# Kernel tuning notes

Measured on AMD Instinct MI355X. Metric: run time of the kernel, lower is better.

The kernel has to match this reference:

```python
import jax, jax.numpy as jnp
import numpy as np

B, N, D = 16, 96, 128
NUM_TOKENS, NUM_CLASSES = 14, 10
NUM_ROUNDS = 5


def setup_inputs() -> dict:
    key = jax.random.key(0)
    ks = jax.random.split(key, 8)
    def lin(k, fan_in, shape):
        return (jax.random.normal(k, shape, jnp.float32) / np.sqrt(fan_in)).astype(jnp.float32)
    return {
        "tok": jax.random.randint(ks[0], (B, N), 0, NUM_TOKENS),
        "A": jax.random.uniform(ks[1], (B, N, N), jnp.float32),
        "embed_W": jax.random.normal(ks[2], (NUM_TOKENS, D), jnp.float32),
        "W1": lin(ks[3], 2 * D, (2 * D, D)),   # msg_fc1, stored [in, out]
        "b1": jnp.zeros((D,), jnp.float32),
        "W2": lin(ks[4], D, (D, D)),           # msg_fc2
        "b2": jnp.zeros((D,), jnp.float32),
        "Wo1": lin(ks[5], D, (D, D)),          # out_fc1
        "bo1": jnp.zeros((D,), jnp.float32),
        "Wo2": lin(ks[6], D, (D, NUM_CLASSES)),  # out_fc2 (no bias)
        "alpha": 0, "tau": 1, "beta": 0, "hard": 0,
    }


def reference(tok, A, embed_W, W1, b1, W2, b2, Wo1, bo1, Wo2, alpha, tau, beta, hard):
    # tok: [B,N] int, A: [B,N,N]. Dropout in eval mode (identity).
    e = embed_W[tok]                      # [B,N,D] token embeddings
    centroids = embed_W[4:]               # [10,D]
    W1e, W1x = W1[:D], W1[D:]             # split of msg_fc1 over the concat [e_i ; x_j]
    e_proj = jnp.einsum('bid,de->bie', e, W1e)  # constant across rounds

    def head(x2d):  # out_fc2(relu(out_fc1(x)))
        return jnp.maximum(x2d @ Wo1 + bo1, 0.0) @ Wo2

    def discretize(x):
        logits = head(x.reshape(-1, D))
        # beta=0, hard=False: gumbel_softmax degenerates to tempered softmax
        a = jax.nn.softmax(logits / tau, axis=-1)
        return (a @ centroids).reshape(x.shape)

    x = e
    for r in range(NUM_ROUNDS):
        xj_proj = jnp.einsum('bjd,de->bje', x, W1x)
        # h[b,i,j] = relu(msg_fc1([e_i ; x_j])) without materializing the concat
        h = jnp.maximum(e_proj[:, :, None, :] + xj_proj[:, None, :, :] + b1, 0.0)  # [B,N,N,D]
        m = jnp.maximum(jnp.einsum('bijd,de->bije', h, W2) + b2, 0.0)
        agg = jnp.einsum('bji,bijd->bid', A, m)  # A^T masked sum over j
        x = x + agg
        if r < NUM_ROUNDS - 1:
            # resid=True, alpha=0 -> np.random.random() > 0 a.s. -> residual add
            x = x + discretize(x)
    out = head(x[:, 0, :])                                  # [B,10]
    x_all = head(x.reshape(-1, D)).reshape(B, N, NUM_CLASSES)  # [B,N,10]
    return out, x_all
```

## Files before the change

kernel.cpp:

```cpp
#include <hip/hip_runtime.h>
#include <hip/hip_bf16.h>
#include <math.h>

#define BB   16
#define NN   96
#define DD   128
#define NCLS 10
#define NTOK 14

typedef __attribute__((ext_vector_type(8))) short bf16x8;
typedef __attribute__((ext_vector_type(8))) unsigned short u16x8;
typedef __attribute__((ext_vector_type(4))) float f32x4;

__device__ __forceinline__ float scalar_as_float(int v) {
    if (v >= -1000000 && v <= 1000000) return (float)v;
    return __int_as_float(v);
}
__device__ __forceinline__ unsigned short f2bf(float f) {
    unsigned u = __float_as_uint(f);
    return (unsigned short)((u + 0x7FFFu + ((u >> 16) & 1u)) >> 16);
}
__device__ __forceinline__ float bf2f(unsigned short h) {
    return __uint_as_float(((unsigned)h) << 16);
}

#define MFMA(A, B, C) __builtin_amdgcn_mfma_f32_16x16x32_bf16(A, B, C, 0, 0, 0)

__global__ __launch_bounds__(256) void k_prep(
    const float* __restrict__ A, const float* __restrict__ embed_W,
    const float* __restrict__ W1, const float* __restrict__ b1,
    const float* __restrict__ W2, const float* __restrict__ b2,
    const float* __restrict__ Wo1,
    float* __restrict__ Mtab, float* __restrict__ t2tab, float* __restrict__ AT,
    unsigned short* __restrict__ w2hi, unsigned short* __restrict__ w1xb,
    unsigned short* __restrict__ wo1b)
{
    const int bx = blockIdx.x;
    const int t  = threadIdx.x;
    const float* W1x = W1 + DD * DD;

    if (bx < NTOK * NTOK) {
        const int ti = bx / NTOK, tj = bx % NTOK;
        const int d = t & 127, half = t >> 7;
        __shared__ float part[2][DD];
        __shared__ unsigned short hb[DD];
        {
            const float* erow  = embed_W + (half ? tj : ti) * DD;
            const float* wbase = half ? W1x : W1;
            float acc = 0.f;
#pragma unroll 8
            for (int k = 0; k < DD; ++k)
                acc = fmaf(erow[k], wbase[k * DD + d], acc);
            part[half][d] = acc;
        }
        __syncthreads();
        if (half == 0) {
            const float v = part[0][d] + b1[d];
            if (tj == 0) t2tab[ti * DD + d] = v;
            hb[d] = f2bf(fmaxf(v + part[1][d], 0.f));
        }
        __syncthreads();
        {
            float m = 0.f;
#pragma unroll 8
            for (int kk = 0; kk < 64; ++kk) {
                const int k = half * 64 + kk;
                m = fmaf(bf2f(hb[k]), bf2f(f2bf(W2[k * DD + d])), m);
            }
            part[half][d] = m;
        }
        __syncthreads();
        if (half == 0)
            Mtab[(ti * NTOK + tj) * DD + d] = fmaxf(part[0][d] + part[1][d] + b2[d], 0.f);
    } else if (bx < 212) {
        const int b = bx - 196;
        __shared__ float tile[NN][NN + 1];
        for (int idx = t; idx < NN * NN; idx += 256)
            tile[idx / NN][idx % NN] = A[b * NN * NN + idx];
        __syncthreads();
        for (int idx = t; idx < NN * NN; idx += 256) {
            const int i = idx / NN, j = idx % NN;
            AT[b * NN * NN + idx] = tile[j][i];
        }
    } else if (bx < 220) {
        const int dt = bx - 212;
        const int kc = t >> 6, ll = t & 63;
        const int base = ((dt * 4 + kc) * 64 + ll) * 8;
        const int c = dt * 16 + (ll & 15);
#pragma unroll
        for (int e = 0; e < 8; ++e)
            w2hi[base + e] = f2bf(W2[(kc * 32 + (ll >> 4) * 8 + e) * DD + c]);
    } else if (bx < 224) {
        const int base = (bx - 220) * 4096 + t * 16;
#pragma unroll
        for (int e = 0; e < 16; ++e) w1xb[base + e] = f2bf(W1x[base + e]);
    } else {
        const int base = (bx - 224) * 4096 + t * 16;
#pragma unroll
        for (int e = 0; e < 16; ++e) wo1b[base + e] = f2bf(Wo1[base + e]);
    }
}

__global__ __launch_bounds__(512, 4) void k_round0(
    const int* __restrict__ tok, const float* __restrict__ AT,
    const float* __restrict__ Mtab, const float* __restrict__ embed_W,
    const unsigned short* __restrict__ wo1b, const float* __restrict__ bo1,
    const float* __restrict__ Wo2, const unsigned short* __restrict__ w1xb,
    const int* __restrict__ tau_p,
    float* __restrict__ x, unsigned short* __restrict__ xj_out)
{
    const int bx = blockIdx.x;
    const int b  = bx >> 5;
    const int is = bx & 31;
    const int t  = threadIdx.x;
    const int w  = t >> 6;
    const int l  = t & 63;
    const int row0 = b * NN + is;

    __shared__ __align__(16) float mt[3][NTOK * DD];
    __shared__ float at3[3][NN];
    __shared__ int   tkj[NN];
    __shared__ float agg_s[3][DD];
    __shared__ float xn_s[3][DD];
    __shared__ float part_s[4][3][DD];

    const int ti0 = tok[row0], ti1 = tok[row0 + 32], ti2 = tok[row0 + 64];
    if (t < NN) {
        tkj[t]    = tok[b * NN + t];
        at3[0][t] = AT[row0 * NN + t];
        at3[1][t] = AT[(row0 + 32) * NN + t];
        at3[2][t] = AT[(row0 + 64) * NN + t];
    }
    for (int idx = t; idx < 3 * NTOK * DD; idx += 512) {
        const int u = idx / (NTOK * DD), rd = idx - u * (NTOK * DD);
        const int tiu = (u == 0) ? ti0 : ((u == 1) ? ti1 : ti2);
        mt[u][rd] = Mtab[tiu * NTOK * DD + rd];
    }
    __syncthreads();

    if (t < 192) {
        const int u = t >> 6, d2 = t & 63;
        const float2* mtu = (const float2*)mt[u];
        float2 acc = {0.f, 0.f};
#pragma unroll 4
        for (int j = 0; j < NN; ++j) {
            const float a = at3[u][j];
            const float2 m = mtu[tkj[j] * 64 + d2];
            acc.x = fmaf(a, m.x, acc.x);
            acc.y = fmaf(a, m.y, acc.y);
        }
        *(float2*)&agg_s[u][d2 * 2] = acc;
    }
    __syncthreads();

    float xr0 = 0.f, xr1 = 0.f;
    if (w < 3) {
        const int tk = (w == 0) ? ti0 : ((w == 1) ? ti1 : ti2);
        xr0 = embed_W[tk * DD + l]      + agg_s[w][l];
        xr1 = embed_W[tk * DD + l + 64] + agg_s[w][l + 64];
        xn_s[w][l]      = xr0;
        xn_s[w][l + 64] = xr1;
    }
    __syncthreads();

    {
        const int q = t >> 7, h = t & 127;
        float p0 = 0.f, p1 = 0.f, p2 = 0.f;
#pragma unroll
        for (int kk = 0; kk < 32; ++kk) {
            const int k = q * 32 + kk;
            const float wv = bf2f(wo1b[k * DD + h]);
            p0 = fmaf(xn_s[0][k], wv, p0);
            p1 = fmaf(xn_s[1][k], wv, p1);
            p2 = fmaf(xn_s[2][k], wv, p2);
        }
        part_s[q][0][h] = p0; part_s[q][1][h] = p1; part_s[q][2][h] = p2;
    }
    __syncthreads();

    if (w < 3) {
        const int row_u = row0 + 32 * w;
        const float hid0 = fmaxf(part_s[0][w][l] + part_s[1][w][l]
                               + part_s[2][w][l] + part_s[3][w][l] + bo1[l], 0.f);
        const float hid1 = fmaxf(part_s[0][w][l + 64] + part_s[1][w][l + 64]
                               + part_s[2][w][l + 64] + part_s[3][w][l + 64] + bo1[l + 64], 0.f);
        float lgp[NCLS];
#pragma unroll
        for (int c = 0; c < NCLS; ++c)
            lgp[c] = hid0 * Wo2[l * NCLS + c] + hid1 * Wo2[(l + 64) * NCLS + c];
#pragma unroll
        for (int s = 1; s < 64; s <<= 1) {
#pragma unroll
            for (int c = 0; c < NCLS; ++c) lgp[c] += __shfl_xor(lgp[c], s);
        }
        float mx = -1e30f;
#pragma unroll
        for (int c = 0; c < NCLS; ++c) mx = fmaxf(mx, lgp[c]);
        const float inv_tau = 1.f / scalar_as_float(tau_p[0]);
        float p[NCLS], den = 0.f;
#pragma unroll
        for (int c = 0; c < NCLS; ++c) { p[c] = expf((lgp[c] - mx) * inv_tau); den += p[c]; }
        const float invden = 1.f / den;
#pragma unroll
        for (int c = 0; c < NCLS; ++c) {
            const float pc = p[c] * invden;
            xr0 = fmaf(pc, embed_W[(4 + c) * DD + l], xr0);
            xr1 = fmaf(pc, embed_W[(4 + c) * DD + l + 64], xr1);
        }
        x[row_u * DD + l]      = xr0;
        x[row_u * DD + l + 64] = xr1;
        xn_s[w][l]      = xr0;
        xn_s[w][l + 64] = xr1;
    }
    __syncthreads();

    {
        const int q = t >> 7, h = t & 127;
        float p0 = 0.f, p1 = 0.f, p2 = 0.f;
#pragma unroll
        for (int kk = 0; kk < 32; ++kk) {
            const int k = q * 32 + kk;
            const float wv = bf2f(w1xb[k * DD + h]);
            p0 = fmaf(xn_s[0][k], wv, p0);
            p1 = fmaf(xn_s[1][k], wv, p1);
            p2 = fmaf(xn_s[2][k], wv, p2);
        }
        part_s[q][0][h] = p0; part_s[q][1][h] = p1; part_s[q][2][h] = p2;
    }
    __syncthreads();

    if (w < 3) {
        const int row_u = row0 + 32 * w;
        xj_out[row_u * DD + l] =
            f2bf(part_s[0][w][l] + part_s[1][w][l] + part_s[2][w][l] + part_s[3][w][l]);
        xj_out[row_u * DD + l + 64] =
            f2bf(part_s[0][w][l + 64] + part_s[1][w][l + 64]
               + part_s[2][w][l + 64] + part_s[3][w][l + 64]);
    }
}

template<int FIN>
__global__ __launch_bounds__(512, 4) void k_round(
    const int* __restrict__ tok, const float* __restrict__ AT,
    const float* __restrict__ t2tab,
    const unsigned short* __restrict__ xj_in,
    const unsigned short* __restrict__ w2hi, const float* __restrict__ b2,
    const float* __restrict__ Wo1, const unsigned short* __restrict__ wo1b,
    const float* __restrict__ bo1, const float* __restrict__ Wo2,
    const float* __restrict__ embed_W, const unsigned short* __restrict__ w1xb,
    const int* __restrict__ tau_p,
    float* __restrict__ x, unsigned short* __restrict__ xj_out,
    float* __restrict__ out, float* __restrict__ x_all)
{
    const int bx = blockIdx.x;
    const int b  = bx >> 5;
    const int is = bx & 31;
    const int t  = threadIdx.x;
    const int w  = t >> 6;
    const int l  = t & 63;
    const int jg  = w >> 2;
    const int dg  = w & 3;
    const int jg3 = jg * 3;
    const int d0 = (t & 15) * 8;
    const int row0 = b * NN + is;

    __shared__ __align__(16) unsigned short hs[2][NN * DD];
    __shared__ float ac_s[2][NN];
    __shared__ float agg_part[3][2][DD];
    __shared__ float xn_s[3][DD];
    __shared__ float part_s[4][3][DD];

    const int tk0 = tok[row0], tk1 = tok[row0 + 32], tk2 = tok[row0 + 64];

    const bf16x8* WH = (const bf16x8*)w2hi;
    const int f0 = (dg * 4) * 64 + l;
    const int f1 = ((dg + 4) * 4) * 64 + l;
    bf16x8 bh00 = WH[f0],        bh10 = WH[f1];
    bf16x8 bh01 = WH[f0 + 64],   bh11 = WH[f1 + 64];
    bf16x8 bh02 = WH[f0 + 128],  bh12 = WH[f1 + 128];
    bf16x8 bh03 = WH[f0 + 192],  bh13 = WH[f1 + 192];
    asm volatile("" : "+v"(bh00), "+v"(bh01), "+v"(bh02), "+v"(bh03),
                      "+v"(bh10), "+v"(bh11), "+v"(bh12), "+v"(bh13));
    const float b2v0 = b2[dg * 16 + (l & 15)];
    const float b2v1 = b2[64 + dg * 16 + (l & 15)];
    const u16x8* xj8 = (const u16x8*)(xj_in + b * NN * DD);

    auto STAGE = [&](int u, int p) {
        const int row_u = row0 + 32 * u;
        const int tk = (u == 0) ? tk0 : ((u == 1) ? tk1 : tk2);
        const float4 ea = *(const float4*)(t2tab + tk * DD + d0);
        const float4 eb = *(const float4*)(t2tab + tk * DD + d0 + 4);
        float v8[8];
        v8[0] = ea.x; v8[1] = ea.y; v8[2] = ea.z; v8[3] = ea.w;
        v8[4] = eb.x; v8[5] = eb.y; v8[6] = eb.z; v8[7] = eb.w;
        if (t < NN) ac_s[p][t] = AT[row_u * NN + t];
#pragma unroll
        for (int it = 0; it < 3; ++it) {
            const int idx8 = t + it * 512;
            const int j = idx8 >> 4;
            const u16x8 xv = xj8[idx8];
            u16x8 hh;
#pragma unroll
            for (int e = 0; e < 8; ++e)
                hh[e] = f2bf(fmaxf(bf2f(xv[e]) + v8[e], 0.f));
            *(u16x8*)&hs[p][(j * DD + d0) ^ ((j & 7) << 3)] = hh;
        }
    };

    auto GEMM = [&](int u, int p) {
        float aggp0 = 0.f, aggp1 = 0.f;
        const unsigned short* hb = hs[p];
#pragma unroll
        for (int jj = 0; jj < 3; ++jj) {
            const int jt  = jg3 + jj;
            const int r16 = jt * 16 + (l & 15);
            const int ko  = (l >> 4) * 8;
            const int sw  = (r16 & 7) << 3;
            const bf16x8 a0 = *(const bf16x8*)&hb[(r16 * DD + ko     ) ^ sw];
            const bf16x8 a1 = *(const bf16x8*)&hb[(r16 * DD + ko + 32) ^ sw];
            const bf16x8 a2 = *(const bf16x8*)&hb[(r16 * DD + ko + 64) ^ sw];
            const bf16x8 a3 = *(const bf16x8*)&hb[(r16 * DD + ko + 96) ^ sw];
            f32x4 c0 = {0.f, 0.f, 0.f, 0.f}, c1 = {0.f, 0.f, 0.f, 0.f};
            c0 = MFMA(a0, bh00, c0);  c1 = MFMA(a0, bh10, c1);
            c0 = MFMA(a1, bh01, c0);  c1 = MFMA(a1, bh11, c1);
            c0 = MFMA(a2, bh02, c0);  c1 = MFMA(a2, bh12, c1);
            c0 = MFMA(a3, bh03, c0);  c1 = MFMA(a3, bh13, c1);
#pragma unroll
            for (int r = 0; r < 4; ++r) {
                const float a = ac_s[p][jt * 16 + (l >> 4) * 4 + r];
                aggp0 = fmaf(a, fmaxf(c0[r] + b2v0, 0.f), aggp0);
                aggp1 = fmaf(a, fmaxf(c1[r] + b2v1, 0.f), aggp1);
            }
        }
        aggp0 += __shfl_xor(aggp0, 16); aggp0 += __shfl_xor(aggp0, 32);
        aggp1 += __shfl_xor(aggp1, 16); aggp1 += __shfl_xor(aggp1, 32);
        if (l < 16) {
            agg_part[u][jg][dg * 16 + l]      = aggp0;
            agg_part[u][jg][64 + dg * 16 + l] = aggp1;
        }
    };

    STAGE(0, 0);
    __syncthreads();
    STAGE(1, 1);
    GEMM(0, 0);
    __syncthreads();
    STAGE(2, 0);
    GEMM(1, 1);
    __syncthreads();
    GEMM(2, 0);
    __syncthreads();

    float xr0 = 0.f, xr1 = 0.f;
    if (w < 3) {
        const int row_u = row0 + 32 * w;
        xr0 = x[row_u * DD + l]      + agg_part[w][0][l]      + agg_part[w][1][l];
        xr1 = x[row_u * DD + l + 64] + agg_part[w][0][l + 64] + agg_part[w][1][l + 64];
        xn_s[w][l]      = xr0;
        xn_s[w][l + 64] = xr1;
    }
    __syncthreads();

    {
        const int q = t >> 7, h = t & 127;
        float p0 = 0.f, p1 = 0.f, p2 = 0.f;
#pragma unroll
        for (int kk = 0; kk < 32; ++kk) {
            const int k = q * 32 + kk;
            const float wv = FIN ? Wo1[k * DD + h] : bf2f(wo1b[k * DD + h]);
            p0 = fmaf(xn_s[0][k], wv, p0);
            p1 = fmaf(xn_s[1][k], wv, p1);
            p2 = fmaf(xn_s[2][k], wv, p2);
        }
        part_s[q][0][h] = p0; part_s[q][1][h] = p1; part_s[q][2][h] = p2;
    }
    __syncthreads();

    if (w < 3) {
        const int row_u = row0 + 32 * w;
        const float hid0 = fmaxf(part_s[0][w][l] + part_s[1][w][l]
                               + part_s[2][w][l] + part_s[3][w][l] + bo1[l], 0.f);
        const float hid1 = fmaxf(part_s[0][w][l + 64] + part_s[1][w][l + 64]
                               + part_s[2][w][l + 64] + part_s[3][w][l + 64] + bo1[l + 64], 0.f);
        float lgp[NCLS];
#pragma unroll
        for (int c = 0; c < NCLS; ++c)
            lgp[c] = hid0 * Wo2[l * NCLS + c] + hid1 * Wo2[(l + 64) * NCLS + c];
#pragma unroll
        for (int s = 1; s < 64; s <<= 1) {
#pragma unroll
            for (int c = 0; c < NCLS; ++c) lgp[c] += __shfl_xor(lgp[c], s);
        }
        if (FIN) {
#pragma unroll
            for (int c = 0; c < NCLS; ++c) {
                if (l == c) {
                    x_all[row_u * NCLS + c] = lgp[c];
                    if (is == 0 && w == 0) out[b * NCLS + c] = lgp[c];
                }
            }
        } else {
            float mx = -1e30f;
#pragma unroll
            for (int c = 0; c < NCLS; ++c) mx = fmaxf(mx, lgp[c]);
            const float inv_tau = 1.f / scalar_as_float(tau_p[0]);
            float p[NCLS], den = 0.f;
#pragma unroll
            for (int c = 0; c < NCLS; ++c) { p[c] = expf((lgp[c] - mx) * inv_tau); den += p[c]; }
            const float invden = 1.f / den;
#pragma unroll
            for (int c = 0; c < NCLS; ++c) {
                const float pc = p[c] * invden;
                xr0 = fmaf(pc, embed_W[(4 + c) * DD + l], xr0);
                xr1 = fmaf(pc, embed_W[(4 + c) * DD + l + 64], xr1);
            }
            x[row_u * DD + l]      = xr0;
            x[row_u * DD + l + 64] = xr1;
            xn_s[w][l]      = xr0;
            xn_s[w][l + 64] = xr1;
        }
    }
    if (FIN) return;
    __syncthreads();

    {
        const int q = t >> 7, h = t & 127;
        float p0 = 0.f, p1 = 0.f, p2 = 0.f;
#pragma unroll
        for (int kk = 0; kk < 32; ++kk) {
            const int k = q * 32 + kk;
            const float wv = bf2f(w1xb[k * DD + h]);
            p0 = fmaf(xn_s[0][k], wv, p0);
            p1 = fmaf(xn_s[1][k], wv, p1);
            p2 = fmaf(xn_s[2][k], wv, p2);
        }
        part_s[q][0][h] = p0; part_s[q][1][h] = p1; part_s[q][2][h] = p2;
    }
    __syncthreads();

    if (w < 3) {
        const int row_u = row0 + 32 * w;
        xj_out[row_u * DD + l] =
            f2bf(part_s[0][w][l] + part_s[1][w][l] + part_s[2][w][l] + part_s[3][w][l]);
        xj_out[row_u * DD + l + 64] =
            f2bf(part_s[0][w][l + 64] + part_s[1][w][l + 64]
               + part_s[2][w][l + 64] + part_s[3][w][l + 64]);
    }
}

extern "C" void kernel_launch(void* const* d_in, const int* in_sizes, int n_in,
                              void* d_out, int out_size, void* d_ws, size_t ws_size,
                              hipStream_t stream)
{
    (void)in_sizes; (void)n_in; (void)out_size; (void)ws_size;
    const int*   tok     = (const int*)d_in[0];
    const float* Aab     = (const float*)d_in[1];
    const float* embed_W = (const float*)d_in[2];
    const float* W1      = (const float*)d_in[3];
    const float* b1      = (const float*)d_in[4];
    const float* W2      = (const float*)d_in[5];
    const float* b2      = (const float*)d_in[6];
    const float* Wo1     = (const float*)d_in[7];
    const float* bo1     = (const float*)d_in[8];
    const float* Wo2     = (const float*)d_in[9];
    const int*   tau_p   = (const int*)d_in[11];

    float* out   = (float*)d_out;
    float* x_all = out + BB * NCLS;

    float* ws     = (float*)d_ws;
    float* x      = ws;
    float* ATr    = ws + BB * NN * DD;
    float* Mtab   = ATr + BB * NN * NN;
    float* t2tab  = Mtab + NTOK * NTOK * DD;
    unsigned short* xjA  = (unsigned short*)(t2tab + NTOK * DD);
    unsigned short* xjB  = xjA + BB * NN * DD;
    unsigned short* w2hi = xjB + BB * NN * DD;
    unsigned short* w1xb = w2hi + DD * DD;
    unsigned short* wo1b = w1xb + DD * DD;

    k_prep<<<228, 256, 0, stream>>>(Aab, embed_W, W1, b1, W2, b2, Wo1,
                                    Mtab, t2tab, ATr, w2hi, w1xb, wo1b);
    k_round0<<<512, 512, 0, stream>>>(tok, ATr, Mtab, embed_W, wo1b, bo1,
                                      Wo2, w1xb, tau_p, x, xjA);
    for (int r = 1; r < 5; ++r) {
        const unsigned short* xin = (r & 1) ? xjA : xjB;
        unsigned short*       xot = (r & 1) ? xjB : xjA;
        if (r < 4)
            k_round<0><<<512, 512, 0, stream>>>(tok, ATr, t2tab, xin, w2hi, b2,
                                                Wo1, wo1b, bo1, Wo2, embed_W, w1xb,
                                                tau_p, x, xot, out, x_all);
        else
            k_round<1><<<512, 512, 0, stream>>>(tok, ATr, t2tab, xin, w2hi, b2,
                                                Wo1, wo1b, bo1, Wo2, embed_W, w1xb,
                                                tau_p, x, xot, out, x_all);
    }
}
```

Baseline: 79.03 us.

## Fold discretize into next-round projection via precomputed centroid-W1x table

Uses linearity: (x + softmax·C)·W1x = x·W1x + softmax·(C·W1x). A new prep block precomputes the centroid projection table, so the head GEMV and the W1x GEMV share one pass over the pre-discretize x. This removes one GEMV pass and two barriers per round. The xj values for a block are also loaded once into registers instead of on every STAGE call, at the cost of extra registers and shared memory, plus small rounding differences from the reordered sums.

New measurement: 86.36 us. 1.09x slower.

```diff
diff --git a/kernel.cpp b/kernel.cpp
--- a/kernel.cpp
+++ b/kernel.cpp
@@ -33,7 +33,7 @@
     const float* __restrict__ Wo1,
     float* __restrict__ Mtab, float* __restrict__ t2tab, float* __restrict__ AT,
     unsigned short* __restrict__ w2hi, unsigned short* __restrict__ w1xb,
-    unsigned short* __restrict__ wo1b)
+    unsigned short* __restrict__ wo1b, float* __restrict__ ctab)
 {
     const int bx = blockIdx.x;
     const int t  = threadIdx.x;
@@ -94,10 +94,29 @@
         const int base = (bx - 220) * 4096 + t * 16;
 #pragma unroll
         for (int e = 0; e < 16; ++e) w1xb[base + e] = f2bf(W1x[base + e]);
+    } else if (bx < 228) {
+        const int base = (bx - 224) * 4096 + t * 16;
+#pragma unroll
+        for (int e = 0; e < 16; ++e) wo1b[base + e] = f2bf(Wo1[base + e]);
     } else {
-        const int base = (bx - 224) * 4096 + t * 16;
-#pragma unroll
-        for (int e = 0; e < 16; ++e) wo1b[base + e] = f2bf(Wo1[base + e]);
+        const int h = t & 127, half = t >> 7;
+        __shared__ float cpart[2][NCLS][DD];
+#pragma unroll
+        for (int c = 0; c < NCLS; ++c) {
+            float acc = 0.f;
+#pragma unroll 8
+            for (int kk = 0; kk < 64; ++kk) {
+                const int k = half * 64 + kk;
+                acc = fmaf(embed_W[(4 + c) * DD + k], bf2f(f2bf(W1x[k * DD + h])), acc);
+            }
+            cpart[half][c][h] = acc;
+        }
+        __syncthreads();
+        if (half == 0) {
+#pragma unroll
+            for (int c = 0; c < NCLS; ++c)
+                ctab[c * DD + h] = cpart[0][c][h] + cpart[1][c][h];
+        }
     }
 }
 
@@ -106,7 +125,7 @@
     const float* __restrict__ Mtab, const float* __restrict__ embed_W,
     const unsigned short* __restrict__ wo1b, const float* __restrict__ bo1,
     const float* __restrict__ Wo2, const unsigned short* __restrict__ w1xb,
-    const int* __restrict__ tau_p,
+    const float* __restrict__ ctab, const int* __restrict__ tau_p,
     float* __restrict__ x, unsigned short* __restrict__ xj_out)
 {
     const int bx = blockIdx.x;
@@ -122,7 +141,8 @@
     __shared__ int   tkj[NN];
     __shared__ float agg_s[3][DD];
     __shared__ float xn_s[3][DD];
-    __shared__ float part_s[4][3][DD];
+    __shared__ float ph_s[4][3][DD];
+    __shared__ float pj_s[4][3][DD];
 
     const int ti0 = tok[row0], ti1 = tok[row0 + 32], ti2 = tok[row0 + 64];
     if (t < NN) {
@@ -165,25 +185,27 @@
 
     {
         const int q = t >> 7, h = t & 127;
-        float p0 = 0.f, p1 = 0.f, p2 = 0.f;
+        float h0 = 0.f, h1 = 0.f, h2 = 0.f, j0 = 0.f, j1 = 0.f, j2 = 0.f;
 #pragma unroll
         for (int kk = 0; kk < 32; ++kk) {
             const int k = q * 32 + kk;
-            const float wv = bf2f(wo1b[k * DD + h]);
-            p0 = fmaf(xn_s[0][k], wv, p0);
-            p1 = fmaf(xn_s[1][k], wv, p1);
-            p2 = fmaf(xn_s[2][k], wv, p2);
-        }
-        part_s[q][0][h] = p0; part_s[q][1][h] = p1; part_s[q][2][h] = p2;
+            const float wo = bf2f(wo1b[k * DD + h]);
+            const float wx = bf2f(w1xb[k * DD + h]);
+            const float x0 = xn_s[0][k], x1 = xn_s[1][k], x2 = xn_s[2][k];
+            h0 = fmaf(x0, wo, h0); h1 = fmaf(x1, wo, h1); h2 = fmaf(x2, wo, h2);
+            j0 = fmaf(x0, wx, j0); j1 = fmaf(x1, wx, j1); j2 = fmaf(x2, wx, j2);
+        }
+        ph_s[q][0][h] = h0; ph_s[q][1][h] = h1; ph_s[q][2][h] = h2;
+        pj_s[q][0][h] = j0; pj_s[q][1][h] = j1; pj_s[q][2][h] = j2;
     }
     __syncthreads();
 
     if (w < 3) {
         const int row_u = row0 + 32 * w;
-        const float hid0 = fmaxf(part_s[0][w][l] + part_s[1][w][l]
-                               + part_s[2][w][l] + part_s[3][w][l] + bo1[l], 0.f);
-        const float hid1 = fmaxf(part_s[0][w][l + 64] + part_s[1][w][l + 64]
-                               + part_s[2][w][l + 64] + part_s[3][w][l + 64] + bo1[l + 64], 0.f);
+        const float hid0 = fmaxf(ph_s[0][w][l] + ph_s[1][w][l]
+                               + ph_s[2][w][l] + ph_s[3][w][l] + bo1[l], 0.f);
+        const float hid1 = fmaxf(ph_s[0][w][l + 64] + ph_s[1][w][l + 64]
+                               + ph_s[2][w][l + 64] + ph_s[3][w][l + 64] + bo1[l + 64], 0.f);
         float lgp[NCLS];
 #pragma unroll
         for (int c = 0; c < NCLS; ++c)
@@ -201,41 +223,21 @@
 #pragma unroll
         for (int c = 0; c < NCLS; ++c) { p[c] = expf((lgp[c] - mx) * inv_tau); den += p[c]; }
         const float invden = 1.f / den;
+        float xj0 = pj_s[0][w][l] + pj_s[1][w][l] + pj_s[2][w][l] + pj_s[3][w][l];
+        float xj1 = pj_s[0][w][l + 64] + pj_s[1][w][l + 64]
+                  + pj_s[2][w][l + 64] + pj_s[3][w][l + 64];
 #pragma unroll
         for (int c = 0; c < NCLS; ++c) {
             const float pc = p[c] * invden;
             xr0 = fmaf(pc, embed_W[(4 + c) * DD + l], xr0);
             xr1 = fmaf(pc, embed_W[(4 + c) * DD + l + 64], xr1);
+            xj0 = fmaf(pc, ctab[c * DD + l], xj0);
+            xj1 = fmaf(pc, ctab[c * DD + l + 64], xj1);
         }
         x[row_u * DD + l]      = xr0;
         x[row_u * DD + l + 64] = xr1;
-        xn_s[w][l]      = xr0;
-        xn_s[w][l + 64] = xr1;
-    }
-    __syncthreads();
-
-    {
-        const int q = t >> 7, h = t & 127;
-        float p0 = 0.f, p1 = 0.f, p2 = 0.f;
-#pragma unroll
-        for (int kk = 0; kk < 32; ++kk) {
-            const int k = q * 32 + kk;
-            const float wv = bf2f(w1xb[k * DD + h]);
-            p0 = fmaf(xn_s[0][k], wv, p0);
-            p1 = fmaf(xn_s[1][k], wv, p1);
-            p2 = fmaf(xn_s[2][k], wv, p2);
-        }
-        part_s[q][0][h] = p0; part_s[q][1][h] = p1; part_s[q][2][h] = p2;
-    }
-    __syncthreads();
-
-    if (w < 3) {
-        const int row_u = row0 + 32 * w;
-        xj_out[row_u * DD + l] =
-            f2bf(part_s[0][w][l] + part_s[1][w][l] + part_s[2][w][l] + part_s[3][w][l]);
-        xj_out[row_u * DD + l + 64] =
-            f2bf(part_s[0][w][l + 64] + part_s[1][w][l + 64]
-               + part_s[2][w][l + 64] + part_s[3][w][l + 64]);
+        xj_out[row_u * DD + l]      = f2bf(xj0);
+        xj_out[row_u * DD + l + 64] = f2bf(xj1);
     }
 }
 
@@ -248,7 +250,7 @@
     const float* __restrict__ Wo1, const unsigned short* __restrict__ wo1b,
     const float* __restrict__ bo1, const float* __restrict__ Wo2,
     const float* __restrict__ embed_W, const unsigned short* __restrict__ w1xb,
-    const int* __restrict__ tau_p,
+    const float* __restrict__ ctab, const int* __restrict__ tau_p,
     float* __restrict__ x, unsigned short* __restrict__ xj_out,
     float* __restrict__ out, float* __restrict__ x_all)
 {
@@ -268,7 +270,8 @@
     __shared__ float ac_s[2][NN];
     __shared__ float agg_part[3][2][DD];
     __shared__ float xn_s[3][DD];
-    __shared__ float part_s[4][3][DD];
+    __shared__ float ph_s[4][3][DD];
+    __shared__ float pj_s[4][3][DD];
 
     const int tk0 = tok[row0], tk1 = tok[row0 + 32], tk2 = tok[row0 + 64];
 
@@ -285,6 +288,11 @@
     const float b2v1 = b2[64 + dg * 16 + (l & 15)];
     const u16x8* xj8 = (const u16x8*)(xj_in + b * NN * DD);
 
+    const u16x8 xva = xj8[t];
+    const u16x8 xvb = xj8[t + 512];
+    const u16x8 xvc = xj8[t + 1024];
+    const int j_a = t >> 4, j_b = (t + 512) >> 4, j_c = (t + 1024) >> 4;
+
     auto STAGE = [&](int u, int p) {
         const int row_u = row0 + 32 * u;
         const int tk = (u == 0) ? tk0 : ((u == 1) ? tk1 : tk2);
@@ -294,17 +302,16 @@
         v8[0] = ea.x; v8[1] = ea.y; v8[2] = ea.z; v8[3] = ea.w;
         v8[4] = eb.x; v8[5] = eb.y; v8[6] = eb.z; v8[7] = eb.w;
         if (t < NN) ac_s[p][t] = AT[row_u * NN + t];
-#pragma unroll
-        for (int it = 0; it < 3; ++it) {
-            const int idx8 = t + it * 512;
-            const int j = idx8 >> 4;
-            const u16x8 xv = xj8[idx8];
-            u16x8 hh;
-#pragma unroll
-            for (int e = 0; e < 8; ++e)
-                hh[e] = f2bf(fmaxf(bf2f(xv[e]) + v8[e], 0.f));
-            *(u16x8*)&hs[p][(j * DD + d0) ^ ((j & 7) << 3)] = hh;
-        }
+        u16x8 hh;
+#pragma unroll
+        for (int e = 0; e < 8; ++e) hh[e] = f2bf(fmaxf(bf2f(xva[e]) + v8[e], 0.f));
+        *(u16x8*)&hs[p][(j_a * DD + d0) ^ ((j_a & 7) << 3)] = hh;
+#pragma unroll
+        for (int e = 0; e < 8; ++e) hh[e] = f2bf(fmaxf(bf2f(xvb[e]) + v8[e], 0.f));
+        *(u16x8*)&hs[p][(j_b * DD + d0) ^ ((j_b & 7) << 3)] = hh;
+#pragma unroll
+        for (int e = 0; e < 8; ++e) hh[e] = f2bf(fmaxf(bf2f(xvc[e]) + v8[e], 0.f));
+        *(u16x8*)&hs[p][(j_c * DD + d0) ^ ((j_c & 7) << 3)] = hh;
     };
 
     auto GEMM = [&](int u, int p) {
@@ -363,25 +370,29 @@
 
     {
         const int q = t >> 7, h = t & 127;
-        float p0 = 0.f, p1 = 0.f, p2 = 0.f;
+        float h0 = 0.f, h1 = 0.f, h2 = 0.f, j0 = 0.f, j1 = 0.f, j2 = 0.f;
 #pragma unroll
         for (int kk = 0; kk < 32; ++kk) {
             const int k = q * 32 + kk;
-            const float wv = FIN ? Wo1[k * DD + h] : bf2f(wo1b[k * DD + h]);
-            p0 = fmaf(xn_s[0][k], wv, p0);
-            p1 = fmaf(xn_s[1][k], wv, p1);
-            p2 = fmaf(xn_s[2][k], wv, p2);
-        }
-        part_s[q][0][h] = p0; part_s[q][1][h] = p1; part_s[q][2][h] = p2;
+            const float wo = FIN ? Wo1[k * DD + h] : bf2f(wo1b[k * DD + h]);
+            const float x0 = xn_s[0][k], x1 = xn_s[1][k], x2 = xn_s[2][k];
+            h0 = fmaf(x0, wo, h0); h1 = fmaf(x1, wo, h1); h2 = fmaf(x2, wo, h2);
+            if (!FIN) {
+                const float wx = bf2f(w1xb[k * DD + h]);
+                j0 = fmaf(x0, wx, j0); j1 = fmaf(x1, wx, j1); j2 = fmaf(x2, wx, j2);
+            }
+        }
+        ph_s[q][0][h] = h0; ph_s[q][1][h] = h1; ph_s[q][2][h] = h2;
+        if (!FIN) { pj_s[q][0][h] = j0; pj_s[q][1][h] = j1; pj_s[q][2][h] = j2; }
     }
     __syncthreads();
 
     if (w < 3) {
         const int row_u = row0 + 32 * w;
-        const float hid0 = fmaxf(part_s[0][w][l] + part_s[1][w][l]
-                               + part_s[2][w][l] + part_s[3][w][l] + bo1[l], 0.f);
-        const float hid1 = fmaxf(part_s[0][w][l + 64] + part_s[1][w][l + 64]
-                               + part_s[2][w][l + 64] + part_s[3][w][l + 64] + bo1[l + 64], 0.f);
+        const float hid0 = fmaxf(ph_s[0][w][l] + ph_s[1][w][l]
+                               + ph_s[2][w][l] + ph_s[3][w][l] + bo1[l], 0.f);
+        const float hid1 = fmaxf(ph_s[0][w][l + 64] + ph_s[1][w][l + 64]
+                               + ph_s[2][w][l + 64] + ph_s[3][w][l + 64] + bo1[l + 64], 0.f);
         float lgp[NCLS];
 #pragma unroll
         for (int c = 0; c < NCLS; ++c)
@@ -408,43 +419,22 @@
 #pragma unroll
             for (int c = 0; c < NCLS; ++c) { p[c] = expf((lgp[c] - mx) * inv_tau); den += p[c]; }
             const float invden = 1.f / den;
+            float xj0 = pj_s[0][w][l] + pj_s[1][w][l] + pj_s[2][w][l] + pj_s[3][w][l];
+            float xj1 = pj_s[0][w][l + 64] + pj_s[1][w][l + 64]
+                      + pj_s[2][w][l + 64] + pj_s[3][w][l + 64];
 #pragma unroll
             for (int c = 0; c < NCLS; ++c) {
                 const float pc = p[c] * invden;
                 xr0 = fmaf(pc, embed_W[(4 + c) * DD + l], xr0);
                 xr1 = fmaf(pc, embed_W[(4 + c) * DD + l + 64], xr1);
+                xj0 = fmaf(pc, ctab[c * DD + l], xj0);
+                xj1 = fmaf(pc, ctab[c * DD + l + 64], xj1);
             }
             x[row_u * DD + l]      = xr0;
             x[row_u * DD + l + 64] = xr1;
-            xn_s[w][l]      = xr0;
-            xn_s[w][l + 64] = xr1;
-        }
-    }
-    if (FIN) return;
-    __syncthreads();
-
-    {
-        const int q = t >> 7, h = t & 127;
-        float p0 = 0.f, p1 = 0.f, p2 = 0.f;
-#pragma unroll
-        for (int kk = 0; kk < 32; ++kk) {
-            const int k = q * 32 + kk;
-            const float wv = bf2f(w1xb[k * DD + h]);
-            p0 = fmaf(xn_s[0][k], wv, p0);
-            p1 = fmaf(xn_s[1][k], wv, p1);
-            p2 = fmaf(xn_s[2][k], wv, p2);
-        }
-        part_s[q][0][h] = p0; part_s[q][1][h] = p1; part_s[q][2][h] = p2;
-    }
-    __syncthreads();
-
-    if (w < 3) {
-        const int row_u = row0 + 32 * w;
-        xj_out[row_u * DD + l] =
-            f2bf(part_s[0][w][l] + part_s[1][w][l] + part_s[2][w][l] + part_s[3][w][l]);
-        xj_out[row_u * DD + l + 64] =
-            f2bf(part_s[0][w][l + 64] + part_s[1][w][l + 64]
-               + part_s[2][w][l + 64] + part_s[3][w][l + 64]);
+            xj_out[row_u * DD + l]      = f2bf(xj0);
+            xj_out[row_u * DD + l + 64] = f2bf(xj1);
+        }
     }
 }
 
@@ -473,26 +463,27 @@
     float* ATr    = ws + BB * NN * DD;
     float* Mtab   = ATr + BB * NN * NN;
     float* t2tab  = Mtab + NTOK * NTOK * DD;
-    unsigned short* xjA  = (unsigned short*)(t2tab + NTOK * DD);
+    float* ctab   = t2tab + NTOK * DD;
+    unsigned short* xjA  = (unsigned short*)(ctab + NCLS * DD);
     unsigned short* xjB  = xjA + BB * NN * DD;
     unsigned short* w2hi = xjB + BB * NN * DD;
     unsigned short* w1xb = w2hi + DD * DD;
     unsigned short* wo1b = w1xb + DD * DD;
 
-    k_prep<<<228, 256, 0, stream>>>(Aab, embed_W, W1, b1, W2, b2, Wo1,
-                                    Mtab, t2tab, ATr, w2hi, w1xb, wo1b);
+    k_prep<<<229, 256, 0, stream>>>(Aab, embed_W, W1, b1, W2, b2, Wo1,
+                                    Mtab, t2tab, ATr, w2hi, w1xb, wo1b, ctab);
     k_round0<<<512, 512, 0, stream>>>(tok, ATr, Mtab, embed_W, wo1b, bo1,
-                                      Wo2, w1xb, tau_p, x, xjA);
+                                      Wo2, w1xb, ctab, tau_p, x, xjA);
     for (int r = 1; r < 5; ++r) {
         const unsigned short* xin = (r & 1) ? xjA : xjB;
         unsigned short*       xot = (r & 1) ? xjB : xjA;
         if (r < 4)
             k_round<0><<<512, 512, 0, stream>>>(tok, ATr, t2tab, xin, w2hi, b2,
                                                 Wo1, wo1b, bo1, Wo2, embed_W, w1xb,
-                                                tau_p, x, xot, out, x_all);
+                                                ctab, tau_p, x, xot, out, x_all);
         else
             k_round<1><<<512, 512, 0, stream>>>(tok, ATr, t2tab, xin, w2hi, b2,
                                                 Wo1, wo1b, bo1, Wo2, embed_W, w1xb,
-                                                tau_p, x, xot, out, x_all);
-    }
-}
+                                                ctab, tau_p, x, xot, out, x_all);
+    }
+}
```
